# Optimization experiments

Measured on AMD Instinct MI355X. Metric: run time of the kernel, lower is better.

## Reference

```python
import jax, jax.numpy as jnp
import numpy as np

B, S, H, V = 128, 2048, 512, 32000


def setup_inputs() -> dict:
    key = jax.random.key(0)
    ks = jax.random.split(key, 12)
    s = 1.0 / np.sqrt(H)
    return {
        "last_token_idx": jax.random.randint(ks[0], (B,), 0, V),
        "last_hidden": jax.random.normal(ks[1], (B, 1, H), jnp.float32),
        "encoder_outputs": jax.random.normal(ks[2], (B, S, H), jnp.float32),
        "embedding": jax.random.normal(ks[3], (V, H), jnp.float32) * 0.02,
        "w_ih": jax.random.uniform(ks[4], (3 * H, H), jnp.float32, -s, s),
        "w_hh": jax.random.uniform(ks[5], (3 * H, H), jnp.float32, -s, s),
        "b_ih": jax.random.uniform(ks[6], (3 * H,), jnp.float32, -s, s),
        "b_hh": jax.random.uniform(ks[7], (3 * H,), jnp.float32, -s, s),
        "W_concat": jax.random.uniform(ks[8], (H, 2 * H), jnp.float32, -s, s),
        "b_concat": jax.random.uniform(ks[9], (H,), jnp.float32, -s, s),
        "W_out": jax.random.uniform(ks[10], (V, H), jnp.float32, -s, s),
        "b_out": jax.random.uniform(ks[11], (V,), jnp.float32, -s, s),
    }


def reference(last_token_idx, last_hidden, encoder_outputs, embedding,
              w_ih, w_hh, b_ih, b_hh, W_concat, b_concat, W_out, b_out):
    # Embedding lookup (dropout_p = 0 -> identity)
    x = embedding[last_token_idx]              # [B, H]
    h = last_hidden[:, 0, :]                   # [B, H]

    # Single-step, single-layer GRU (PyTorch gate order: r, z, n)
    gi = x @ w_ih.T + b_ih                     # [B, 3H]
    gh = h @ w_hh.T + b_hh                     # [B, 3H]
    gi_r, gi_z, gi_n = jnp.split(gi, 3, axis=1)
    gh_r, gh_z, gh_n = jnp.split(gh, 3, axis=1)
    r = jax.nn.sigmoid(gi_r + gh_r)
    z = jax.nn.sigmoid(gi_z + gh_z)
    n = jnp.tanh(gi_n + r * gh_n)
    h_new = (1.0 - z) * n + z * h              # [B, H] (= decoder_output)

    # Dot attention (vectorized form of the per-(b,i) python loop)
    energies = jnp.einsum("bh,bsh->bs", h_new, encoder_outputs)  # [B, S]
    attn = jax.nn.softmax(energies, axis=-1)                      # [B, S]
    context = jnp.einsum("bs,bsh->bh", attn, encoder_outputs)     # [B, H]

    concat_out = jnp.tanh(jnp.concatenate([h_new, context], axis=1) @ W_concat.T + b_concat)
    output = concat_out @ W_out.T + b_out      # [B, V]

    return output, h_new[:, None, :], attn[:, :, None]
```

## Files before the change

### kernel.cpp

```cpp
#include <hip/hip_runtime.h>
#include <math.h>

#define B_ 128
#define S_ 2048
#define H_ 512
#define V_ 32000
#define NCH 8
#define NW 4
#define NP (NCH * NW)

typedef __attribute__((ext_vector_type(8))) short bf16x8;
typedef __attribute__((ext_vector_type(4))) float f32x4;

__device__ __forceinline__ short f2bf(float f) {
  union { float f; unsigned u; } v;
  v.f = f;
  unsigned r = v.u + 0x7fffu + ((v.u >> 16) & 1u);
  return (short)(r >> 16);
}
__device__ __forceinline__ float bf2f(short s) {
  union { unsigned u; float f; } v;
  v.u = ((unsigned)(unsigned short)s) << 16;
  return v.f;
}

template <int BM, int BN, int BK, int TM, int TN, int ACT>
__device__ __forceinline__ void gemm_body(
    const float* __restrict__ A, const int* __restrict__ arows,
    const float* __restrict__ Bm, const float* __restrict__ bias,
    float* __restrict__ C, int M, int N, int K, int bx, int by) {
  __shared__ float As[BK][BM + 4];
  __shared__ float Bs[BK][BN + 4];
  const int tid = threadIdx.x;
  const int tx = tid % (BN / TN);
  const int ty = tid / (BN / TN);
  const int n0 = bx * BN;
  const int m0 = by * BM;

  float acc[TM][TN];
#pragma unroll
  for (int i = 0; i < TM; i++)
#pragma unroll
    for (int j = 0; j < TN; j++) acc[i][j] = 0.f;

  for (int k0 = 0; k0 < K; k0 += BK) {
#pragma unroll
    for (int e = tid; e < BM * BK; e += 256) {
      int m = e / BK, kk = e % BK;
      int row = arows ? arows[m0 + m] : (m0 + m);
      As[kk][m] = A[(long)row * K + k0 + kk];
    }
#pragma unroll
    for (int e = tid; e < BN * BK; e += 256) {
      int n = e / BK, kk = e % BK;
      Bs[kk][n] = Bm[(long)(n0 + n) * K + k0 + kk];
    }
    __syncthreads();
#pragma unroll
    for (int kk = 0; kk < BK; kk++) {
      float av[TM], bv[TN];
#pragma unroll
      for (int i = 0; i < TM; i++) av[i] = As[kk][ty * TM + i];
#pragma unroll
      for (int j = 0; j < TN; j++) bv[j] = Bs[kk][tx * TN + j];
#pragma unroll
      for (int i = 0; i < TM; i++)
#pragma unroll
        for (int j = 0; j < TN; j++) acc[i][j] = fmaf(av[i], bv[j], acc[i][j]);
    }
    __syncthreads();
  }

#pragma unroll
  for (int i = 0; i < TM; i++) {
    int m = m0 + ty * TM + i;
#pragma unroll
    for (int j = 0; j < TN; j++) {
      int n = n0 + tx * TN + j;
      float c = acc[i][j] + bias[n];
      if (ACT == 1) c = tanhf(c);
      C[(long)m * N + n] = c;
    }
  }
}

template <int BM, int BN, int BK, int TM, int TN, int ACT>
__global__ __launch_bounds__(256) void gemm_tn(
    const float* __restrict__ A, const int* __restrict__ arows,
    const float* __restrict__ Bm, const float* __restrict__ bias,
    float* __restrict__ C, int M, int N, int K) {
  gemm_body<BM, BN, BK, TM, TN, ACT>(A, arows, Bm, bias, C, M, N, K,
                                     blockIdx.x, blockIdx.y);
}

__global__ __launch_bounds__(256) void gru_gates(
    const float* __restrict__ emb, const int* __restrict__ idx,
    const float* __restrict__ hlast, const float* __restrict__ w_ih,
    const float* __restrict__ w_hh, const float* __restrict__ b_ih,
    const float* __restrict__ b_hh, float* __restrict__ gi,
    float* __restrict__ gh) {
  if (blockIdx.z == 0)
    gemm_body<32, 32, 16, 2, 2, 0>(emb, idx, w_ih, b_ih, gi, B_, 3 * H_, H_,
                                   blockIdx.x, blockIdx.y);
  else
    gemm_body<32, 32, 16, 2, 2, 0>(hlast, nullptr, w_hh, b_hh, gh, B_, 3 * H_,
                                   H_, blockIdx.x, blockIdx.y);
}

__global__ __launch_bounds__(256) void gemm_mfma_split(
    const float* __restrict__ A, const float* __restrict__ Bm,
    const float* __restrict__ bias, float* __restrict__ C, int M, int N,
    int K) {
  __shared__ __align__(16) short Ah[64][72];
  __shared__ __align__(16) short Al[64][72];
  __shared__ __align__(16) short Bh[128][72];
  __shared__ __align__(16) short Bl[128][72];

  const int tid = threadIdx.x;
  const int wv = tid >> 6;
  const int lane = tid & 63;
  const int m0 = blockIdx.y * 64;
  const int n0 = blockIdx.x * 128;

  f32x4 acc[4][2];
#pragma unroll
  for (int i = 0; i < 4; i++)
#pragma unroll
    for (int j = 0; j < 2; j++) acc[i][j] = (f32x4){0.f, 0.f, 0.f, 0.f};

  const int ar = tid >> 2;
  const int ac = (tid & 3) << 4;
  const int br = tid >> 1;
  const int bc = (tid & 1) << 5;

  const int rr = lane & 15;
  const int kg = (lane >> 4) << 3;

  for (int k0 = 0; k0 < K; k0 += 64) {
    {
      const float4* src = (const float4*)(A + (long)(m0 + ar) * K + k0 + ac);
      float4 fv[4];
#pragma unroll
      for (int q = 0; q < 4; q++) fv[q] = src[q];
#pragma unroll
      for (int q = 0; q < 2; q++) {
        float4 u = fv[2 * q], w = fv[2 * q + 1];
        float x[8] = {u.x, u.y, u.z, u.w, w.x, w.y, w.z, w.w};
        bf16x8 hh, ll;
#pragma unroll
        for (int j = 0; j < 8; j++) {
          short h = f2bf(x[j]);
          hh[j] = h;
          ll[j] = f2bf(x[j] - bf2f(h));
        }
        *(bf16x8*)&Ah[ar][ac + q * 8] = hh;
        *(bf16x8*)&Al[ar][ac + q * 8] = ll;
      }
    }
    {
      const float4* src = (const float4*)(Bm + (long)(n0 + br) * K + k0 + bc);
      float4 fv[8];
#pragma unroll
      for (int q = 0; q < 8; q++) fv[q] = src[q];
#pragma unroll
      for (int q = 0; q < 4; q++) {
        float4 u = fv[2 * q], w = fv[2 * q + 1];
        float x[8] = {u.x, u.y, u.z, u.w, w.x, w.y, w.z, w.w};
        bf16x8 hh, ll;
#pragma unroll
        for (int j = 0; j < 8; j++) {
          short h = f2bf(x[j]);
          hh[j] = h;
          ll[j] = f2bf(x[j] - bf2f(h));
        }
        *(bf16x8*)&Bh[br][bc + q * 8] = hh;
        *(bf16x8*)&Bl[br][bc + q * 8] = ll;
      }
    }
    __syncthreads();

#pragma unroll
    for (int ks = 0; ks < 2; ks++) {
      const int kb = ks * 32 + kg;
      bf16x8 a_h[4], a_l[4], b_h[2], b_l[2];
#pragma unroll
      for (int i = 0; i < 4; i++) {
        a_h[i] = *(const bf16x8*)&Ah[i * 16 + rr][kb];
        a_l[i] = *(const bf16x8*)&Al[i * 16 + rr][kb];
      }
#pragma unroll
      for (int j = 0; j < 2; j++) {
        b_h[j] = *(const bf16x8*)&Bh[wv * 32 + j * 16 + rr][kb];
        b_l[j] = *(const bf16x8*)&Bl[wv * 32 + j * 16 + rr][kb];
      }
#pragma unroll
      for (int i = 0; i < 4; i++)
#pragma unroll
        for (int j = 0; j < 2; j++) {
          acc[i][j] = __builtin_amdgcn_mfma_f32_16x16x32_bf16(
              a_h[i], b_h[j], acc[i][j], 0, 0, 0);
          acc[i][j] = __builtin_amdgcn_mfma_f32_16x16x32_bf16(
              a_h[i], b_l[j], acc[i][j], 0, 0, 0);
          acc[i][j] = __builtin_amdgcn_mfma_f32_16x16x32_bf16(
              a_l[i], b_h[j], acc[i][j], 0, 0, 0);
        }
    }
    __syncthreads();
  }

  const int rg = lane >> 4;
#pragma unroll
  for (int i = 0; i < 4; i++) {
#pragma unroll
    for (int j = 0; j < 2; j++) {
      int col = n0 + wv * 32 + j * 16 + rr;
      float bv = bias[col];
#pragma unroll
      for (int r = 0; r < 4; r++) {
        int row = m0 + i * 16 + rg * 4 + r;
        C[(long)row * N + col] = acc[i][j][r] + bv;
      }
    }
  }
}

__global__ __launch_bounds__(256) void gru_ew(
    const float* __restrict__ gi, const float* __restrict__ gh,
    const float* __restrict__ hlast, float* __restrict__ hnew,
    float* __restrict__ cin) {
  int idx = blockIdx.x * 256 + threadIdx.x;
  int b = idx >> 9, j = idx & 511;
  const float* gib = gi + b * 1536;
  const float* ghb = gh + b * 1536;
  float gir = gib[j], giz = gib[512 + j], gin = gib[1024 + j];
  float ghr = ghb[j], ghz = ghb[512 + j], ghn = ghb[1024 + j];
  float r = 1.f / (1.f + __expf(-(gir + ghr)));
  float z = 1.f / (1.f + __expf(-(giz + ghz)));
  float n = tanhf(gin + r * ghn);
  float h = (1.f - z) * n + z * hlast[idx];
  hnew[idx] = h;
  cin[b * 1024 + j] = h;
}

__global__ __launch_bounds__(256) void attn_partial(
    const float* __restrict__ enc, const float* __restrict__ hnew,
    float* __restrict__ energies, float* __restrict__ pm,
    float* __restrict__ pl, float* __restrict__ pacc) {
  const int bid = blockIdx.x;
  const int b = bid >> 3;
  const int c = bid & (NCH - 1);
  const int wave = threadIdx.x >> 6;
  const int lane = threadIdx.x & 63;

  const float4* hp = (const float4*)(hnew + b * H_);
  const float4 hA = hp[lane];
  const float4 hB = hp[64 + lane];

  float m = -INFINITY, l = 0.f;
  float4 aA = {0.f, 0.f, 0.f, 0.f}, aB = {0.f, 0.f, 0.f, 0.f};
  float my_e = 0.f;
  const int s0 = c * 256 + wave * 64;

#pragma unroll 2
  for (int i = 0; i < 64; ++i) {
    int s = s0 + i;
    const float4* ep = (const float4*)(enc + ((long)b * S_ + s) * H_);
    float4 eA = ep[lane];
    float4 eB = ep[64 + lane];
    float v = eA.x * hA.x + eA.y * hA.y + eA.z * hA.z + eA.w * hA.w +
              eB.x * hB.x + eB.y * hB.y + eB.z * hB.z + eB.w * hB.w;
#pragma unroll
    for (int off = 32; off > 0; off >>= 1) v += __shfl_xor(v, off);
    if (lane == i) my_e = v;
    float mn = fmaxf(m, v);
    float sc = __expf(m - mn);
    float p = __expf(v - mn);
    m = mn;
    l = l * sc + p;
    aA.x = aA.x * sc + p * eA.x;
    aA.y = aA.y * sc + p * eA.y;
    aA.z = aA.z * sc + p * eA.z;
    aA.w = aA.w * sc + p * eA.w;
    aB.x = aB.x * sc + p * eB.x;
    aB.y = aB.y * sc + p * eB.y;
    aB.z = aB.z * sc + p * eB.z;
    aB.w = aB.w * sc + p * eB.w;
  }

  energies[(long)b * S_ + s0 + lane] = my_e;
  int pidx = b * NP + c * NW + wave;
  if (lane == 0) {
    pm[pidx] = m;
    pl[pidx] = l;
  }
  float4* pa = (float4*)(pacc + (long)pidx * H_);
  pa[lane] = aA;
  pa[64 + lane] = aB;
}

__global__ __launch_bounds__(256) void attn_combine(
    const float* __restrict__ energies, const float* __restrict__ pm,
    const float* __restrict__ pl, const float* __restrict__ pacc,
    float* __restrict__ attn, float* __restrict__ cin) {
  const int b = blockIdx.x;
  const int tid = threadIdx.x;

  float m_b = -INFINITY;
#pragma unroll
  for (int i = 0; i < NP; i++) m_b = fmaxf(m_b, pm[b * NP + i]);
  float wgt[NP];
  float l_b = 0.f;
#pragma unroll
  for (int i = 0; i < NP; i++) {
    wgt[i] = __expf(pm[b * NP + i] - m_b);
    l_b += pl[b * NP + i] * wgt[i];
  }
  float inv = 1.f / l_b;

  for (int k = tid; k < H_; k += 256) {
    float s = 0.f;
#pragma unroll
    for (int i = 0; i < NP; i++)
      s += pacc[(long)(b * NP + i) * H_ + k] * wgt[i];
    cin[b * 1024 + 512 + k] = s * inv;
  }
  for (int s = tid; s < S_; s += 256) {
    attn[(long)b * S_ + s] = __expf(energies[(long)b * S_ + s] - m_b) * inv;
  }
}

extern "C" void kernel_launch(void* const* d_in, const int* in_sizes, int n_in,
                              void* d_out, int out_size, void* d_ws,
                              size_t ws_size, hipStream_t stream) {
  const int* idx = (const int*)d_in[0];
  const float* hlast = (const float*)d_in[1];
  const float* enc = (const float*)d_in[2];
  const float* emb = (const float*)d_in[3];
  const float* w_ih = (const float*)d_in[4];
  const float* w_hh = (const float*)d_in[5];
  const float* b_ih = (const float*)d_in[6];
  const float* b_hh = (const float*)d_in[7];
  const float* W_cat = (const float*)d_in[8];
  const float* b_cat = (const float*)d_in[9];
  const float* W_out = (const float*)d_in[10];
  const float* b_out = (const float*)d_in[11];

  float* out = (float*)d_out;
  float* out_h = out + (long)B_ * V_;
  float* out_a = out_h + B_ * H_;

  float* ws = (float*)d_ws;
  float* gi = ws;
  float* gh = gi + B_ * 3 * H_;
  float* en = gh + B_ * 3 * H_;
  float* pm = en + (long)B_ * S_;
  float* pl = pm + B_ * NP;
  float* pacc = pl + B_ * NP;
  float* cin = pacc + (long)B_ * NP * H_;
  float* cout = cin + B_ * 2 * H_;

  dim3 blk(256);
  gru_gates<<<dim3(1536 / 32, 128 / 32, 2), blk, 0, stream>>>(
      emb, idx, hlast, w_ih, w_hh, b_ih, b_hh, gi, gh);
  gru_ew<<<dim3(B_ * H_ / 256), blk, 0, stream>>>(gi, gh, hlast, out_h, cin);
  attn_partial<<<dim3(B_ * NCH), blk, 0, stream>>>(enc, out_h, en, pm, pl,
                                                   pacc);
  attn_combine<<<dim3(B_), blk, 0, stream>>>(en, pm, pl, pacc, out_a, cin);
  gemm_tn<16, 32, 16, 1, 2, 1><<<dim3(512 / 32, 128 / 16), blk, 0, stream>>>(
      cin, nullptr, W_cat, b_cat, cout, B_, H_, 2 * H_);
  gemm_mfma_split<<<dim3(V_ / 128, B_ / 64), blk, 0, stream>>>(
      cout, W_out, b_out, out, B_, V_, H_);
}
```

Measured before the change: 895.9 us.

## Vectorize and prefetch GEMM tiles, cover all rows per block, unroll attention

The generic SIMT GEMM now loads tiles as float4 into registers and prefetches the next K tile while computing the current one, with BK raised to 64. The MFMA output GEMM now covers all 128 batch rows in one block with a 2x2 wave layout, so each W_out tile is read and split to bf16 once instead of twice. It also prefetches the B tile into registers and sets launch_bounds(256,2). The attention partial kernel processes two sequence positions per iteration to raise memory-level parallelism. The costs are higher register pressure and larger shared memory use, which may reduce occupancy.

```diff
diff --git a/kernel.cpp b/kernel.cpp
--- a/kernel.cpp
+++ b/kernel.cpp
@@ -29,14 +29,39 @@
     const float* __restrict__ A, const int* __restrict__ arows,
     const float* __restrict__ Bm, const float* __restrict__ bias,
     float* __restrict__ C, int M, int N, int K, int bx, int by) {
-  __shared__ float As[BK][BM + 4];
-  __shared__ float Bs[BK][BN + 4];
+  __shared__ __align__(16) float As[BK][BM + 2];
+  __shared__ __align__(16) float Bs[BK][BN + 2];
+  constexpr int KF4 = BK / 4;
+  constexpr int NA = BM * KF4 / 256;
+  constexpr int NB = BN * KF4 / 256;
   const int tid = threadIdx.x;
   const int tx = tid % (BN / TN);
   const int ty = tid / (BN / TN);
   const int n0 = bx * BN;
   const int m0 = by * BM;
 
+  int aRow[NA];
+#pragma unroll
+  for (int q = 0; q < NA; q++) {
+    int ch = tid + 256 * q;
+    int r = ch / KF4;
+    aRow[q] = arows ? arows[m0 + r] : (m0 + r);
+  }
+
+  float4 ra[NA], rb[NB];
+#pragma unroll
+  for (int q = 0; q < NA; q++) {
+    int ch = tid + 256 * q;
+    int c = ch % KF4;
+    ra[q] = *(const float4*)(A + (long)aRow[q] * K + 4 * c);
+  }
+#pragma unroll
+  for (int q = 0; q < NB; q++) {
+    int ch = tid + 256 * q;
+    int r = ch / KF4, c = ch % KF4;
+    rb[q] = *(const float4*)(Bm + (long)(n0 + r) * K + 4 * c);
+  }
+
   float acc[TM][TN];
 #pragma unroll
   for (int i = 0; i < TM; i++)
@@ -45,17 +70,38 @@
 
   for (int k0 = 0; k0 < K; k0 += BK) {
 #pragma unroll
-    for (int e = tid; e < BM * BK; e += 256) {
-      int m = e / BK, kk = e % BK;
-      int row = arows ? arows[m0 + m] : (m0 + m);
-      As[kk][m] = A[(long)row * K + k0 + kk];
-    }
-#pragma unroll
-    for (int e = tid; e < BN * BK; e += 256) {
-      int n = e / BK, kk = e % BK;
-      Bs[kk][n] = Bm[(long)(n0 + n) * K + k0 + kk];
+    for (int q = 0; q < NA; q++) {
+      int ch = tid + 256 * q;
+      int r = ch / KF4, c = ch % KF4;
+      As[4 * c + 0][r] = ra[q].x;
+      As[4 * c + 1][r] = ra[q].y;
+      As[4 * c + 2][r] = ra[q].z;
+      As[4 * c + 3][r] = ra[q].w;
+    }
+#pragma unroll
+    for (int q = 0; q < NB; q++) {
+      int ch = tid + 256 * q;
+      int r = ch / KF4, c = ch % KF4;
+      Bs[4 * c + 0][r] = rb[q].x;
+      Bs[4 * c + 1][r] = rb[q].y;
+      Bs[4 * c + 2][r] = rb[q].z;
+      Bs[4 * c + 3][r] = rb[q].w;
     }
     __syncthreads();
+    if (k0 + BK < K) {
+#pragma unroll
+      for (int q = 0; q < NA; q++) {
+        int ch = tid + 256 * q;
+        int c = ch % KF4;
+        ra[q] = *(const float4*)(A + (long)aRow[q] * K + k0 + BK + 4 * c);
+      }
+#pragma unroll
+      for (int q = 0; q < NB; q++) {
+        int ch = tid + 256 * q;
+        int r = ch / KF4, c = ch % KF4;
+        rb[q] = *(const float4*)(Bm + (long)(n0 + r) * K + k0 + BK + 4 * c);
+      }
+    }
 #pragma unroll
     for (int kk = 0; kk < BK; kk++) {
       float av[TM], bv[TN];
@@ -100,51 +146,55 @@
     const float* __restrict__ b_hh, float* __restrict__ gi,
     float* __restrict__ gh) {
   if (blockIdx.z == 0)
-    gemm_body<32, 32, 16, 2, 2, 0>(emb, idx, w_ih, b_ih, gi, B_, 3 * H_, H_,
+    gemm_body<32, 32, 64, 2, 2, 0>(emb, idx, w_ih, b_ih, gi, B_, 3 * H_, H_,
                                    blockIdx.x, blockIdx.y);
   else
-    gemm_body<32, 32, 16, 2, 2, 0>(hlast, nullptr, w_hh, b_hh, gh, B_, 3 * H_,
+    gemm_body<32, 32, 64, 2, 2, 0>(hlast, nullptr, w_hh, b_hh, gh, B_, 3 * H_,
                                    H_, blockIdx.x, blockIdx.y);
 }
 
-__global__ __launch_bounds__(256) void gemm_mfma_split(
+__global__ __launch_bounds__(256, 2) void gemm_mfma_split(
     const float* __restrict__ A, const float* __restrict__ Bm,
-    const float* __restrict__ bias, float* __restrict__ C, int M, int N,
-    int K) {
-  __shared__ __align__(16) short Ah[64][72];
-  __shared__ __align__(16) short Al[64][72];
+    const float* __restrict__ bias, float* __restrict__ C, int N, int K) {
+  __shared__ __align__(16) short Ah[128][72];
+  __shared__ __align__(16) short Al[128][72];
   __shared__ __align__(16) short Bh[128][72];
   __shared__ __align__(16) short Bl[128][72];
 
   const int tid = threadIdx.x;
   const int wv = tid >> 6;
   const int lane = tid & 63;
-  const int m0 = blockIdx.y * 64;
   const int n0 = blockIdx.x * 128;
-
-  f32x4 acc[4][2];
-#pragma unroll
-  for (int i = 0; i < 4; i++)
-#pragma unroll
-    for (int j = 0; j < 2; j++) acc[i][j] = (f32x4){0.f, 0.f, 0.f, 0.f};
-
-  const int ar = tid >> 2;
-  const int ac = (tid & 3) << 4;
-  const int br = tid >> 1;
-  const int bc = (tid & 1) << 5;
+  const int wm = (wv >> 1) * 64;
+  const int wn = (wv & 1) * 64;
+
+  const int sr = tid >> 1;
+  const int sc = (tid & 1) << 5;
 
   const int rr = lane & 15;
   const int kg = (lane >> 4) << 3;
+  const int rg = lane >> 4;
+
+  f32x4 acc[4][4];
+#pragma unroll
+  for (int i = 0; i < 4; i++)
+#pragma unroll
+    for (int j = 0; j < 4; j++) acc[i][j] = (f32x4){0.f, 0.f, 0.f, 0.f};
+
+  float4 fb[8];
+#pragma unroll
+  for (int q = 0; q < 8; q++)
+    fb[q] = *(const float4*)(Bm + (long)(n0 + sr) * K + sc + 4 * q);
 
   for (int k0 = 0; k0 < K; k0 += 64) {
     {
-      const float4* src = (const float4*)(A + (long)(m0 + ar) * K + k0 + ac);
-      float4 fv[4];
-#pragma unroll
-      for (int q = 0; q < 4; q++) fv[q] = src[q];
-#pragma unroll
-      for (int q = 0; q < 2; q++) {
-        float4 u = fv[2 * q], w = fv[2 * q + 1];
+      float4 fa[8];
+#pragma unroll
+      for (int q = 0; q < 8; q++)
+        fa[q] = *(const float4*)(A + (long)sr * K + k0 + sc + 4 * q);
+#pragma unroll
+      for (int g = 0; g < 4; g++) {
+        float4 u = fa[2 * g], w = fa[2 * g + 1];
         float x[8] = {u.x, u.y, u.z, u.w, w.x, w.y, w.z, w.w};
         bf16x8 hh, ll;
 #pragma unroll
@@ -153,50 +203,51 @@
           hh[j] = h;
           ll[j] = f2bf(x[j] - bf2f(h));
         }
-        *(bf16x8*)&Ah[ar][ac + q * 8] = hh;
-        *(bf16x8*)&Al[ar][ac + q * 8] = ll;
-      }
-    }
-    {
-      const float4* src = (const float4*)(Bm + (long)(n0 + br) * K + k0 + bc);
-      float4 fv[8];
-#pragma unroll
-      for (int q = 0; q < 8; q++) fv[q] = src[q];
-#pragma unroll
-      for (int q = 0; q < 4; q++) {
-        float4 u = fv[2 * q], w = fv[2 * q + 1];
-        float x[8] = {u.x, u.y, u.z, u.w, w.x, w.y, w.z, w.w};
-        bf16x8 hh, ll;
-#pragma unroll
-        for (int j = 0; j < 8; j++) {
-          short h = f2bf(x[j]);
-          hh[j] = h;
-          ll[j] = f2bf(x[j] - bf2f(h));
-        }
-        *(bf16x8*)&Bh[br][bc + q * 8] = hh;
-        *(bf16x8*)&Bl[br][bc + q * 8] = ll;
-      }
+        *(bf16x8*)&Ah[sr][sc + 8 * g] = hh;
+        *(bf16x8*)&Al[sr][sc + 8 * g] = ll;
+      }
+    }
+#pragma unroll
+    for (int g = 0; g < 4; g++) {
+      float4 u = fb[2 * g], w = fb[2 * g + 1];
+      float x[8] = {u.x, u.y, u.z, u.w, w.x, w.y, w.z, w.w};
+      bf16x8 hh, ll;
+#pragma unroll
+      for (int j = 0; j < 8; j++) {
+        short h = f2bf(x[j]);
+        hh[j] = h;
+        ll[j] = f2bf(x[j] - bf2f(h));
+      }
+      *(bf16x8*)&Bh[sr][sc + 8 * g] = hh;
+      *(bf16x8*)&Bl[sr][sc + 8 * g] = ll;
     }
     __syncthreads();
+
+    if (k0 + 64 < K) {
+#pragma unroll
+      for (int q = 0; q < 8; q++)
+        fb[q] =
+            *(const float4*)(Bm + (long)(n0 + sr) * K + k0 + 64 + sc + 4 * q);
+    }
 
 #pragma unroll
     for (int ks = 0; ks < 2; ks++) {
       const int kb = ks * 32 + kg;
-      bf16x8 a_h[4], a_l[4], b_h[2], b_l[2];
+      bf16x8 a_h[4], a_l[4], b_h[4], b_l[4];
 #pragma unroll
       for (int i = 0; i < 4; i++) {
-        a_h[i] = *(const bf16x8*)&Ah[i * 16 + rr][kb];
-        a_l[i] = *(const bf16x8*)&Al[i * 16 + rr][kb];
-      }
-#pragma unroll
-      for (int j = 0; j < 2; j++) {
-        b_h[j] = *(const bf16x8*)&Bh[wv * 32 + j * 16 + rr][kb];
-        b_l[j] = *(const bf16x8*)&Bl[wv * 32 + j * 16 + rr][kb];
+        a_h[i] = *(const bf16x8*)&Ah[wm + i * 16 + rr][kb];
+        a_l[i] = *(const bf16x8*)&Al[wm + i * 16 + rr][kb];
+      }
+#pragma unroll
+      for (int j = 0; j < 4; j++) {
+        b_h[j] = *(const bf16x8*)&Bh[wn + j * 16 + rr][kb];
+        b_l[j] = *(const bf16x8*)&Bl[wn + j * 16 + rr][kb];
       }
 #pragma unroll
       for (int i = 0; i < 4; i++)
 #pragma unroll
-        for (int j = 0; j < 2; j++) {
+        for (int j = 0; j < 4; j++) {
           acc[i][j] = __builtin_amdgcn_mfma_f32_16x16x32_bf16(
               a_h[i], b_h[j], acc[i][j], 0, 0, 0);
           acc[i][j] = __builtin_amdgcn_mfma_f32_16x16x32_bf16(
@@ -208,17 +259,16 @@
     __syncthreads();
   }
 
-  const int rg = lane >> 4;
 #pragma unroll
   for (int i = 0; i < 4; i++) {
 #pragma unroll
-    for (int j = 0; j < 2; j++) {
-      int col = n0 + wv * 32 + j * 16 + rr;
-      float bv = bias[col];
+    for (int j = 0; j < 4; j++) {
+      int col = n0 + wn + j * 16 + rr;
+      float bvv = bias[col];
 #pragma unroll
       for (int r = 0; r < 4; r++) {
-        int row = m0 + i * 16 + rg * 4 + r;
-        C[(long)row * N + col] = acc[i][j][r] + bv;
+        int row = wm + i * 16 + rg * 4 + r;
+        C[(long)row * N + col] = acc[i][j][r] + bvv;
       }
     }
   }
@@ -262,29 +312,40 @@
   const int s0 = c * 256 + wave * 64;
 
 #pragma unroll 2
-  for (int i = 0; i < 64; ++i) {
-    int s = s0 + i;
-    const float4* ep = (const float4*)(enc + ((long)b * S_ + s) * H_);
-    float4 eA = ep[lane];
-    float4 eB = ep[64 + lane];
-    float v = eA.x * hA.x + eA.y * hA.y + eA.z * hA.z + eA.w * hA.w +
-              eB.x * hB.x + eB.y * hB.y + eB.z * hB.z + eB.w * hB.w;
-#pragma unroll
-    for (int off = 32; off > 0; off >>= 1) v += __shfl_xor(v, off);
-    if (lane == i) my_e = v;
-    float mn = fmaxf(m, v);
+  for (int i = 0; i < 32; ++i) {
+    int s = s0 + 2 * i;
+    const float4* ep0 = (const float4*)(enc + ((long)b * S_ + s) * H_);
+    const float4* ep1 = (const float4*)(enc + ((long)b * S_ + s + 1) * H_);
+    float4 e0A = ep0[lane];
+    float4 e0B = ep0[64 + lane];
+    float4 e1A = ep1[lane];
+    float4 e1B = ep1[64 + lane];
+    float v0 = e0A.x * hA.x + e0A.y * hA.y + e0A.z * hA.z + e0A.w * hA.w +
+               e0B.x * hB.x + e0B.y * hB.y + e0B.z * hB.z + e0B.w * hB.w;
+    float v1 = e1A.x * hA.x + e1A.y * hA.y + e1A.z * hA.z + e1A.w * hA.w +
+               e1B.x * hB.x + e1B.y * hB.y + e1B.z * hB.z + e1B.w * hB.w;
+#pragma unroll
+    for (int off = 32; off > 0; off >>= 1) {
+      v0 += __shfl_xor(v0, off);
+      v1 += __shfl_xor(v1, off);
+    }
+    if (lane == 2 * i) my_e = v0;
+    if (lane == 2 * i + 1) my_e = v1;
+    float mx = fmaxf(v0, v1);
+    float mn = fmaxf(m, mx);
     float sc = __expf(m - mn);
-    float p = __expf(v - mn);
+    float p0 = __expf(v0 - mn);
+    float p1 = __expf(v1 - mn);
     m = mn;
-    l = l * sc + p;
-    aA.x = aA.x * sc + p * eA.x;
-    aA.y = aA.y * sc + p * eA.y;
-    aA.z = aA.z * sc + p * eA.z;
-    aA.w = aA.w * sc + p * eA.w;
-    aB.x = aB.x * sc + p * eB.x;
-    aB.y = aB.y * sc + p * eB.y;
-    aB.z = aB.z * sc + p * eB.z;
-    aB.w = aB.w * sc + p * eB.w;
+    l = l * sc + p0 + p1;
+    aA.x = fmaf(p1, e1A.x, fmaf(p0, e0A.x, aA.x * sc));
+    aA.y = fmaf(p1, e1A.y, fmaf(p0, e0A.y, aA.y * sc));
+    aA.z = fmaf(p1, e1A.z, fmaf(p0, e0A.z, aA.z * sc));
+    aA.w = fmaf(p1, e1A.w, fmaf(p0, e0A.w, aA.w * sc));
+    aB.x = fmaf(p1, e1B.x, fmaf(p0, e0B.x, aB.x * sc));
+    aB.y = fmaf(p1, e1B.y, fmaf(p0, e0B.y, aB.y * sc));
+    aB.z = fmaf(p1, e1B.z, fmaf(p0, e0B.z, aB.z * sc));
+    aB.w = fmaf(p1, e1B.w, fmaf(p0, e0B.w, aB.w * sc));
   }
 
   energies[(long)b * S_ + s0 + lane] = my_e;
@@ -366,8 +427,8 @@
   attn_partial<<<dim3(B_ * NCH), blk, 0, stream>>>(enc, out_h, en, pm, pl,
                                                    pacc);
   attn_combine<<<dim3(B_), blk, 0, stream>>>(en, pm, pl, pacc, out_a, cin);
-  gemm_tn<16, 32, 16, 1, 2, 1><<<dim3(512 / 32, 128 / 16), blk, 0, stream>>>(
+  gemm_tn<16, 32, 64, 1, 2, 1><<<dim3(512 / 32, 128 / 16), blk, 0, stream>>>(
       cin, nullptr, W_cat, b_cat, cout, B_, H_, 2 * H_);
-  gemm_mfma_split<<<dim3(V_ / 128, B_ / 64), blk, 0, stream>>>(
-      cout, W_out, b_out, out, B_, V_, H_);
-}
+  gemm_mfma_split<<<dim3(V_ / 128), blk, 0, stream>>>(cout, W_out, b_out, out,
+                                                      V_, H_);
+}
```

Measured after the change: 837.1 us. 1.07x faster.
